# Performance work log

Measured on AMD Instinct MI355X. Metric: run time of the kernel, lower is better.

## Reference

```python
import jax, jax.numpy as jnp
import numpy as np

B, C, F_, T = 32, 2, 1024, 512
CF = C * F_
H = 128  # lstm hidden / embedding dim


def setup_inputs() -> dict:
    key = jax.random.key(0)
    ks = jax.random.split(key, 12)
    s = 0.05
    return {
        "x": jax.random.normal(ks[0], (B, C, F_, T), dtype=jnp.float32),
        "W_fc1": jax.random.normal(ks[1], (H, CF), dtype=jnp.float32) * s,
        "b_fc1": jax.random.normal(ks[2], (H,), dtype=jnp.float32) * s,
        "Wih_f": jax.random.normal(ks[3], (4 * H, H), dtype=jnp.float32) * s,
        "Whh_f": jax.random.normal(ks[4], (4 * H, H), dtype=jnp.float32) * s,
        "b_f": jax.random.normal(ks[5], (4 * H,), dtype=jnp.float32) * s,
        "Wih_b": jax.random.normal(ks[6], (4 * H, H), dtype=jnp.float32) * s,
        "Whh_b": jax.random.normal(ks[7], (4 * H, H), dtype=jnp.float32) * s,
        "b_b": jax.random.normal(ks[8], (4 * H,), dtype=jnp.float32) * s,
        "W_out": jax.random.normal(ks[9], (H, 2 * H), dtype=jnp.float32) * s,
        "b_out": jax.random.normal(ks[10], (H,), dtype=jnp.float32) * s,
    }


def _lstm_scan(x, Wih, Whh, b):
    # x: (L, T, H); recurrence over L (torch treats the (B,128) input as an
    # unbatched sequence of length B), vectorized over the T frames.
    L, Tn, _ = x.shape
    Hn = Whh.shape[1]

    def step(carry, xt):
        h, c = carry  # (T, H)
        z = xt @ Wih.T + h @ Whh.T + b  # (T, 4H)
        i, f, g, o = jnp.split(z, 4, axis=-1)
        c = jax.nn.sigmoid(f) * c + jax.nn.sigmoid(i) * jnp.tanh(g)
        h = jax.nn.sigmoid(o) * jnp.tanh(c)
        return (h, c), h

    init = (jnp.zeros((Tn, Hn), x.dtype), jnp.zeros((Tn, Hn), x.dtype))
    _, hs = jax.lax.scan(step, init, x)
    return hs  # (L, T, H)


def reference(x, W_fc1, b_fc1, Wih_f, Whh_f, b_f, Wih_b, Whh_b, b_b, W_out, b_out):
    Bn, Cn, Fn, Tn = x.shape
    # fc1 applied per time frame: (B, CF, T) -> (B, T, 128)
    xr = x.reshape(Bn, Cn * Fn, Tn).transpose(0, 2, 1)
    h = jnp.einsum("btc,dc->btd", xr, W_fc1) + b_fc1
    # bidirectional LSTM over the batch axis (torch unbatched-input semantics)
    hf = _lstm_scan(h, Wih_f, Whh_f, b_f)
    hb = _lstm_scan(h[::-1], Wih_b, Whh_b, b_b)[::-1]
    hs = jnp.concatenate([hf, hb], axis=-1)  # (B, T, 256)
    out = jnp.einsum("btd,ed->bte", hs, W_out) + b_out  # (B, T, 128)
    return out.transpose(0, 2, 1)  # (B, 128, T), matching torch.stack(dim=2)
```

## Files before the change

kernel.cpp:

```cpp
#include <hip/hip_runtime.h>
#include <stdint.h>

typedef __attribute__((ext_vector_type(8))) short short8;
typedef __attribute__((ext_vector_type(4))) float floatx4;

__device__ __forceinline__ float bf16_to_f(uint16_t u) {
    union { uint32_t i; float f; } v; v.i = ((uint32_t)u) << 16; return v.f;
}
__device__ __forceinline__ uint16_t f_to_bf16(float f) {
    union { uint32_t i; float f; } v; v.f = f;
    uint32_t u = v.i;
    u += 0x7FFFu + ((u >> 16) & 1u);
    return (uint16_t)(u >> 16);
}
__device__ __forceinline__ void gload16(const void* g, void* l) {
    __builtin_amdgcn_global_load_lds(
        (const __attribute__((address_space(1))) void*)g,
        (__attribute__((address_space(3))) void*)l, 16, 0, 0);
}
__device__ __forceinline__ float rcpf(float x) { return __builtin_amdgcn_rcpf(x); }

__device__ __forceinline__ void bar_lds() {
    asm volatile("s_waitcnt lgkmcnt(0)" ::: "memory");
    __builtin_amdgcn_s_barrier();
    asm volatile("" ::: "memory");
}

#define B_  32
#define T_  512
#define CF_ 2048
#define H_  128
#define G4_ 512
#define BT_ 16384
#define LOG2E 1.4426950408889634f

__global__ __launch_bounds__(256) void k_cvt_all(
        const float* __restrict__ Wfc, const float* __restrict__ Wih_f,
        const float* __restrict__ Wih_b, const float* __restrict__ Whh_f,
        const float* __restrict__ Whh_b, const float* __restrict__ Wout,
        uint16_t* __restrict__ WswzB, uint16_t* __restrict__ WihB,
        uint16_t* __restrict__ WhhB, uint16_t* __restrict__ WoutB) {
    const int blk = blockIdx.x;
    if (blk < 256) {
        const int i = blk * 1024 + threadIdx.x * 4;
        const int d = i >> 11, k = i & 2047;
        float4 v = *(const float4*)&Wfc[i];
        ushort4 o;
        o.x = f_to_bf16(v.x); o.y = f_to_bf16(v.y);
        o.z = f_to_bf16(v.z); o.w = f_to_bf16(v.w);
        const int kc = k >> 5, lk = (k >> 3) & 3, e = k & 7;
        const int mf = d >> 4, lm = d & 15;
        *(ushort4*)&WswzB[(size_t)(((kc * 8 + mf) * 64 + lk * 16 + lm) * 8 + e)] = o;
        return;
    }
    const float* s; uint16_t* d; int off;
    if (blk < 320)      { s = Wih_f; d = WihB;          off = blk - 256; }
    else if (blk < 384) { s = Wih_b; d = WihB + 65536;  off = blk - 320; }
    else if (blk < 448) { s = Whh_f; d = WhhB;          off = blk - 384; }
    else if (blk < 512) { s = Whh_b; d = WhhB + 65536;  off = blk - 448; }
    else                { s = Wout;  d = WoutB;         off = blk - 512; }
    const int i = off * 1024 + threadIdx.x * 4;
    float4 v = *(const float4*)&s[i];
    ushort4 o;
    o.x = f_to_bf16(v.x); o.y = f_to_bf16(v.y);
    o.z = f_to_bf16(v.z); o.w = f_to_bf16(v.w);
    *(ushort4*)&d[i] = o;
}

__global__ __launch_bounds__(256) void k_fc1w(const float* __restrict__ x,
                                              const uint16_t* __restrict__ Wswz,
                                              float* __restrict__ Hpart) {
    const int tid = threadIdx.x, w = tid >> 6, l = tid & 63;
    const int lm = l & 15, lk = l >> 4;
    const int bt0 = blockIdx.x * 16;
    const int bb = bt0 >> 9, t0 = bt0 & 511;
    const int kc4 = w;
    const float* xb = x + ((size_t)bb * CF_ + kc4 * 512) * T_ + t0 + lm;

    floatx4 acc[8] = {};
    #pragma unroll 2
    for (int s = 0; s < 16; ++s) {
        const int kk = s * 32;
        float xv[8];
        #pragma unroll
        for (int j = 0; j < 8; ++j)
            xv[j] = xb[(size_t)(kk + lk * 8 + j) * T_];
        short8 bfr;
        #pragma unroll
        for (int j = 0; j < 8; ++j)
            bfr[j] = (short)f_to_bf16(xv[j]);
        const uint16_t* wp = Wswz + ((size_t)(kc4 * 16 + s) * 8 * 64 + l) * 8;
        #pragma unroll
        for (int mf = 0; mf < 8; ++mf) {
            short8 a = *(const short8*)(wp + mf * 512);
            acc[mf] = __builtin_amdgcn_mfma_f32_16x16x32_bf16(a, bfr, acc[mf], 0, 0, 0);
        }
    }
    float* Hp = Hpart + (size_t)kc4 * H_ * BT_;
    #pragma unroll
    for (int mf = 0; mf < 8; ++mf) {
        const int d0 = mf * 16 + lk * 4;
        #pragma unroll
        for (int r = 0; r < 4; ++r)
            Hp[(size_t)(d0 + r) * BT_ + bt0 + lm] = acc[mf][r];
    }
}

__global__ __launch_bounds__(256) void k_hsum(const float* __restrict__ Hpart,
                                              const float* __restrict__ bfc,
                                              uint16_t* __restrict__ Hcm) {
    const int d = blockIdx.y, bt = blockIdx.x * 1024 + threadIdx.x * 4;
    const float b = bfc[d];
    float4 s = *(const float4*)&Hpart[(size_t)d * BT_ + bt];
    #pragma unroll
    for (int kc = 1; kc < 4; ++kc) {
        const float4 v = *(const float4*)&Hpart[(size_t)kc * H_ * BT_ + (size_t)d * BT_ + bt];
        s.x += v.x; s.y += v.y; s.z += v.z; s.w += v.w;
    }
    uint16_t* o = Hcm + ((size_t)(d >> 3) * BT_ + bt) * 8 + (d & 7);
    o[0]  = f_to_bf16(s.x + b);
    o[8]  = f_to_bf16(s.y + b);
    o[16] = f_to_bf16(s.z + b);
    o[24] = f_to_bf16(s.w + b);
}

__global__ __launch_bounds__(256) void k_xproj(const uint16_t* __restrict__ Hcm,
                                               const uint16_t* __restrict__ WihB,
                                               const float* __restrict__ b_f,
                                               const float* __restrict__ b_b,
                                               uint16_t* __restrict__ Xp) {
    __shared__ __align__(16) uint16_t As[64 * 136];
    __shared__ __align__(16) uint16_t Bs[16 * 66 * 8];
    const int bt0 = blockIdx.x * 64, gy = blockIdx.y;
    const int dir = gy >> 3;
    const int gl0 = gy * 64 - dir * 512;
    const int tid = threadIdx.x, w = tid >> 6, l = tid & 63;
    const int lm = l & 15, lk = l >> 4;

    #pragma unroll
    for (int j = 0; j < 4; ++j) {
        const int c = w * 4 + j;
        gload16(Hcm + ((size_t)c * BT_ + bt0 + l) * 8, Bs + (c * 66 + l) * 8);
    }
    {
        const int r = tid >> 2, c4 = tid & 3;
        const uint16_t* src = WihB + (size_t)(gy * 64 + r) * H_ + c4 * 32;
        short8 v0 = *(const short8*)(src);
        short8 v1 = *(const short8*)(src + 8);
        short8 v2 = *(const short8*)(src + 16);
        short8 v3 = *(const short8*)(src + 24);
        uint16_t* dst = &As[r * 136 + c4 * 32];
        *(short8*)(dst)      = v0;
        *(short8*)(dst + 8)  = v1;
        *(short8*)(dst + 16) = v2;
        *(short8*)(dst + 24) = v3;
    }
    __syncthreads();

    const int wm = (w >> 1) * 32, wn = (w & 1) * 32;
    short8 a[2][4], bfr[2][4];
    #pragma unroll
    for (int kf = 0; kf < 4; ++kf) {
        #pragma unroll
        for (int mf = 0; mf < 2; ++mf)
            a[mf][kf] = *(const short8*)&As[(wm + mf * 16 + lm) * 136 + kf * 32 + lk * 8];
        #pragma unroll
        for (int nf = 0; nf < 2; ++nf)
            bfr[nf][kf] = *(const short8*)&Bs[((kf * 4 + lk) * 66 + wn + nf * 16 + lm) * 8];
    }
    floatx4 acc[2][2] = {};
    #pragma unroll
    for (int kf = 0; kf < 4; ++kf)
        #pragma unroll
        for (int mf = 0; mf < 2; ++mf)
            #pragma unroll
            for (int nf = 0; nf < 2; ++nf)
                acc[mf][nf] = __builtin_amdgcn_mfma_f32_16x16x32_bf16(a[mf][kf], bfr[nf][kf], acc[mf][nf], 0, 0, 0);

    const float* bi = dir ? b_b : b_f;
    #pragma unroll
    for (int mf = 0; mf < 2; ++mf) {
        const int g = gl0 + wm + mf * 16 + lk * 4;
        const float4 bv = *(const float4*)&bi[g];
        #pragma unroll
        for (int nf = 0; nf < 2; ++nf) {
            const int bt = bt0 + wn + nf * 16 + lm;
            const int bb = bt >> 9, t = bt & 511;
            ushort4 o;
            o.x = f_to_bf16(acc[mf][nf][0] + bv.x);
            o.y = f_to_bf16(acc[mf][nf][1] + bv.y);
            o.z = f_to_bf16(acc[mf][nf][2] + bv.z);
            o.w = f_to_bf16(acc[mf][nf][3] + bv.w);
            *(ushort4*)&Xp[((size_t)(dir * B_ + bb) * T_ + t) * G4_ + g] = o;
        }
    }
}

__global__ __launch_bounds__(512) void k_lstm(const uint16_t* __restrict__ Xp,
                                              const uint16_t* __restrict__ WhhB,
                                              uint16_t* __restrict__ hs) {
    __shared__ __align__(16) uint16_t h_sh[2][16 * 136];
    const int dir = blockIdx.y, t0 = blockIdx.x * 16;
    const int tid = threadIdx.x, w = tid >> 6, l = tid & 63;
    const int lm = l & 15, lk = l >> 4;
    const int gcol = w * 16 + lm;
    const int tloc = lk * 4;
    const uint16_t* Wp = WhhB + dir * (G4_ * H_);

    short8 bw[4][4];
    #pragma unroll
    for (int q = 0; q < 4; ++q)
        #pragma unroll
        for (int kf = 0; kf < 4; ++kf)
            bw[q][kf] = *(const short8*)&Wp[(size_t)(q * H_ + gcol) * H_ + kf * 32 + lk * 8];

    for (int i = tid; i < 16 * 136; i += 512) h_sh[0][i] = 0;
    float c[4] = {0.f, 0.f, 0.f, 0.f};

    uint16_t xva[4][4], xvb[4][4];
    {
        const int b0 = dir ? (B_ - 1) : 0;
        const uint16_t* xp = Xp + ((size_t)(dir * B_ + b0) * T_ + t0 + tloc) * G4_;
        #pragma unroll
        for (int r = 0; r < 4; ++r)
            #pragma unroll
            for (int q = 0; q < 4; ++q)
                xva[r][q] = xp[(size_t)r * G4_ + q * H_ + gcol];
    }
    bar_lds();

    auto step = [&](int s, uint16_t (&xc)[4][4], uint16_t (&xn)[4][4], int par) {
        const int b_idx = dir ? (B_ - 1 - s) : s;
        short8 af[4];
        #pragma unroll
        for (int kf = 0; kf < 4; ++kf)
            af[kf] = *(const short8*)&h_sh[par][lm * 136 + kf * 32 + lk * 8];
        floatx4 acc[4] = {};
        #pragma unroll
        for (int q = 0; q < 4; ++q)
            #pragma unroll
            for (int kf = 0; kf < 4; ++kf)
                acc[q] = __builtin_amdgcn_mfma_f32_16x16x32_bf16(af[kf], bw[q][kf], acc[q], 0, 0, 0);
        if (s < B_ - 1) {
            const int bn = dir ? (B_ - 2 - s) : (s + 1);
            const uint16_t* xp = Xp + ((size_t)(dir * B_ + bn) * T_ + t0 + tloc) * G4_;
            #pragma unroll
            for (int r = 0; r < 4; ++r)
                #pragma unroll
                for (int q = 0; q < 4; ++q)
                    xn[r][q] = xp[(size_t)r * G4_ + q * H_ + gcol];
        }
        #pragma unroll
        for (int r = 0; r < 4; ++r) {
            float zi = acc[0][r] + bf16_to_f(xc[r][0]);
            float zf = acc[1][r] + bf16_to_f(xc[r][1]);
            float zg = acc[2][r] + bf16_to_f(xc[r][2]);
            float zo = acc[3][r] + bf16_to_f(xc[r][3]);
            float si = rcpf(1.f + __builtin_amdgcn_exp2f(-LOG2E * zi));
            float sf = rcpf(1.f + __builtin_amdgcn_exp2f(-LOG2E * zf));
            float so = rcpf(1.f + __builtin_amdgcn_exp2f(-LOG2E * zo));
            float tg = 1.f - 2.f * rcpf(1.f + __builtin_amdgcn_exp2f(2.f * LOG2E * zg));
            c[r] = sf * c[r] + si * tg;
            float tc = 1.f - 2.f * rcpf(1.f + __builtin_amdgcn_exp2f(2.f * LOG2E * c[r]));
            float hn = so * tc;
            uint16_t hb = f_to_bf16(hn);
            h_sh[par ^ 1][(tloc + r) * 136 + gcol] = hb;
            hs[((size_t)b_idx * T_ + t0 + tloc + r) * 256 + dir * H_ + gcol] = hb;
        }
        bar_lds();
    };

    for (int s2 = 0; s2 < 16; ++s2) {
        step(2 * s2,     xva, xvb, 0);
        step(2 * s2 + 1, xvb, xva, 1);
    }
}

__global__ __launch_bounds__(256) void k_outm(const uint16_t* __restrict__ WoutB,
                                              const uint16_t* __restrict__ hs,
                                              const float* __restrict__ bout,
                                              float* __restrict__ out) {
    __shared__ __align__(16) uint16_t As[4096], Bs[4096];
    const int b = blockIdx.z, m0 = blockIdx.y * 64, n0 = blockIdx.x * 64;
    const int tid = threadIdx.x, w = tid >> 6, l = tid & 63;
    const int wm = (w >> 1) * 32, wn = (w & 1) * 32;
    const int lm = l & 15, lk = l >> 4;
    const uint16_t* A = WoutB + (size_t)m0 * 256;
    const uint16_t* Bp = hs + ((size_t)b * T_ + n0) * 256;
    floatx4 acc[2][2] = {};
    const uint16_t* gA = A + (size_t)l * 256;
    const uint16_t* gB = Bp + (size_t)l * 256;
    for (int k0 = 0; k0 < 256; k0 += 64) {
        __syncthreads();
        gload16(gA + k0 + (2 * w) * 8,     As + ((2 * w) * 64 + l) * 8);
        gload16(gA + k0 + (2 * w + 1) * 8, As + ((2 * w + 1) * 64 + l) * 8);
        gload16(gB + k0 + (2 * w) * 8,     Bs + ((2 * w) * 64 + l) * 8);
        gload16(gB + k0 + (2 * w + 1) * 8, Bs + ((2 * w + 1) * 64 + l) * 8);
        __syncthreads();
        short8 a[2][2], bfr[2][2];
        #pragma unroll
        for (int kf = 0; kf < 2; ++kf) {
            #pragma unroll
            for (int mf = 0; mf < 2; ++mf)
                a[mf][kf] = *(const short8*)&As[((kf * 4 + lk) * 64 + wm + mf * 16 + lm) * 8];
            #pragma unroll
            for (int nf = 0; nf < 2; ++nf)
                bfr[nf][kf] = *(const short8*)&Bs[((kf * 4 + lk) * 64 + wn + nf * 16 + lm) * 8];
        }
        #pragma unroll
        for (int mf = 0; mf < 2; ++mf)
            #pragma unroll
            for (int nf = 0; nf < 2; ++nf) {
                acc[mf][nf] = __builtin_amdgcn_mfma_f32_16x16x32_bf16(a[mf][0], bfr[nf][0], acc[mf][nf], 0, 0, 0);
                acc[mf][nf] = __builtin_amdgcn_mfma_f32_16x16x32_bf16(a[mf][1], bfr[nf][1], acc[mf][nf], 0, 0, 0);
            }
    }
    #pragma unroll
    for (int mf = 0; mf < 2; ++mf) {
        const int e0 = m0 + wm + mf * 16 + lk * 4;
        const float4 bv = *(const float4*)&bout[e0];
        #pragma unroll
        for (int nf = 0; nf < 2; ++nf) {
            const int t = n0 + wn + nf * 16 + lm;
            out[((size_t)b * H_ + e0 + 0) * T_ + t] = acc[mf][nf][0] + bv.x;
            out[((size_t)b * H_ + e0 + 1) * T_ + t] = acc[mf][nf][1] + bv.y;
            out[((size_t)b * H_ + e0 + 2) * T_ + t] = acc[mf][nf][2] + bv.z;
            out[((size_t)b * H_ + e0 + 3) * T_ + t] = acc[mf][nf][3] + bv.w;
        }
    }
}

extern "C" void kernel_launch(void* const* d_in, const int* in_sizes, int n_in,
                              void* d_out, int out_size, void* d_ws, size_t ws_size,
                              hipStream_t stream) {
    const float* x     = (const float*)d_in[0];
    const float* Wfc   = (const float*)d_in[1];
    const float* bfc   = (const float*)d_in[2];
    const float* Wih_f = (const float*)d_in[3];
    const float* Whh_f = (const float*)d_in[4];
    const float* b_f   = (const float*)d_in[5];
    const float* Wih_b = (const float*)d_in[6];
    const float* Whh_b = (const float*)d_in[7];
    const float* b_b   = (const float*)d_in[8];
    const float* Wout  = (const float*)d_in[9];
    const float* bout  = (const float*)d_in[10];
    float* out = (float*)d_out;

    char* ws = (char*)d_ws;
    uint16_t* Xp    = (uint16_t*)(ws);
    uint16_t* hsB   = (uint16_t*)(ws + 33554432);
    float*    Hpart = (float*)   (ws + 41943040);
    uint16_t* Hcm   = (uint16_t*)(ws + 75497472);
    uint16_t* Wswz  = (uint16_t*)(ws + 79691776);
    uint16_t* WihB  = (uint16_t*)(ws + 80216064);
    uint16_t* WhhB  = (uint16_t*)(ws + 80478208);
    uint16_t* WoutB = (uint16_t*)(ws + 80740352);

    k_cvt_all<<<dim3(544), 256, 0, stream>>>(Wfc, Wih_f, Wih_b, Whh_f, Whh_b, Wout,
                                             Wswz, WihB, WhhB, WoutB);
    k_fc1w <<<dim3(1024),     256, 0, stream>>>(x, Wswz, Hpart);
    k_hsum <<<dim3(16, 128),  256, 0, stream>>>(Hpart, bfc, Hcm);
    k_xproj<<<dim3(256, 16),  256, 0, stream>>>(Hcm, WihB, b_f, b_b, Xp);
    k_lstm <<<dim3(32, 2),    512, 0, stream>>>(Xp, WhhB, hsB);
    k_outm <<<dim3(8, 2, 32), 256, 0, stream>>>(WoutB, hsB, bout, out);
}
```

Measured before the change: 332.5 us.

## Stage fc1 weight slices in LDS and widen per-wave time tile

The fc1 GEMM kernel now gives each block a 256-deep K-slice (8 splits) across 256 time frames. The block's 64KB bf16 weight slice is staged in LDS, and each wave computes 4 time fragments so every weight fragment feeds 4 MFMAs. The old kernel re-read weights from global memory for every 16-frame block. The cost is a larger partial-sum buffer (8 splits instead of 4) for the reduction kernel to sum, plus heavy LDS and register use (128 accumulator floats), which lowers occupancy.

```diff
diff --git a/kernel.cpp b/kernel.cpp
--- a/kernel.cpp
+++ b/kernel.cpp
@@ -67,42 +67,57 @@
     *(ushort4*)&d[i] = o;
 }
 
-__global__ __launch_bounds__(256) void k_fc1w(const float* __restrict__ x,
-                                              const uint16_t* __restrict__ Wswz,
-                                              float* __restrict__ Hpart) {
+__global__ __launch_bounds__(256) void k_fc1w2(const float* __restrict__ x,
+                                               const uint16_t* __restrict__ Wswz,
+                                               float* __restrict__ Hpart) {
+    __shared__ __align__(16) uint16_t Wl[32768];
     const int tid = threadIdx.x, w = tid >> 6, l = tid & 63;
     const int lm = l & 15, lk = l >> 4;
-    const int bt0 = blockIdx.x * 16;
+    const int bt0 = blockIdx.x * 256;
+    const int kc8 = blockIdx.y;
     const int bb = bt0 >> 9, t0 = bt0 & 511;
-    const int kc4 = w;
-    const float* xb = x + ((size_t)bb * CF_ + kc4 * 512) * T_ + t0 + lm;
-
-    floatx4 acc[8] = {};
+    const int btw = w * 64;
+
+    const uint16_t* wsrc = Wswz + (size_t)kc8 * 32768;
+    #pragma unroll
+    for (int it = 0; it < 16; ++it)
+        gload16(wsrc + (size_t)(it * 256 + tid) * 8, Wl + (it * 256 + tid) * 8);
+    __syncthreads();
+
+    const float* xb = x + ((size_t)bb * CF_ + kc8 * 256) * T_ + t0 + btw + lm;
+
+    floatx4 acc[8][4] = {};
     #pragma unroll 2
-    for (int s = 0; s < 16; ++s) {
+    for (int s = 0; s < 8; ++s) {
         const int kk = s * 32;
-        float xv[8];
-        #pragma unroll
-        for (int j = 0; j < 8; ++j)
-            xv[j] = xb[(size_t)(kk + lk * 8 + j) * T_];
-        short8 bfr;
-        #pragma unroll
-        for (int j = 0; j < 8; ++j)
-            bfr[j] = (short)f_to_bf16(xv[j]);
-        const uint16_t* wp = Wswz + ((size_t)(kc4 * 16 + s) * 8 * 64 + l) * 8;
+        short8 bfr[4];
+        #pragma unroll
+        for (int nf = 0; nf < 4; ++nf) {
+            float xv[8];
+            #pragma unroll
+            for (int j = 0; j < 8; ++j)
+                xv[j] = xb[(size_t)(kk + lk * 8 + j) * T_ + nf * 16];
+            #pragma unroll
+            for (int j = 0; j < 8; ++j)
+                bfr[nf][j] = (short)f_to_bf16(xv[j]);
+        }
         #pragma unroll
         for (int mf = 0; mf < 8; ++mf) {
-            short8 a = *(const short8*)(wp + mf * 512);
-            acc[mf] = __builtin_amdgcn_mfma_f32_16x16x32_bf16(a, bfr, acc[mf], 0, 0, 0);
-        }
-    }
-    float* Hp = Hpart + (size_t)kc4 * H_ * BT_;
+            const short8 a = *(const short8*)&Wl[((s * 8 + mf) * 64 + l) * 8];
+            #pragma unroll
+            for (int nf = 0; nf < 4; ++nf)
+                acc[mf][nf] = __builtin_amdgcn_mfma_f32_16x16x32_bf16(a, bfr[nf], acc[mf][nf], 0, 0, 0);
+        }
+    }
+    float* Hp = Hpart + (size_t)kc8 * H_ * BT_;
     #pragma unroll
     for (int mf = 0; mf < 8; ++mf) {
         const int d0 = mf * 16 + lk * 4;
         #pragma unroll
-        for (int r = 0; r < 4; ++r)
-            Hp[(size_t)(d0 + r) * BT_ + bt0 + lm] = acc[mf][r];
+        for (int nf = 0; nf < 4; ++nf)
+            #pragma unroll
+            for (int r = 0; r < 4; ++r)
+                Hp[(size_t)(d0 + r) * BT_ + bt0 + btw + nf * 16 + lm] = acc[mf][nf][r];
     }
 }
 
@@ -113,7 +128,7 @@
     const float b = bfc[d];
     float4 s = *(const float4*)&Hpart[(size_t)d * BT_ + bt];
     #pragma unroll
-    for (int kc = 1; kc < 4; ++kc) {
+    for (int kc = 1; kc < 8; ++kc) {
         const float4 v = *(const float4*)&Hpart[(size_t)kc * H_ * BT_ + (size_t)d * BT_ + bt];
         s.x += v.x; s.y += v.y; s.z += v.z; s.w += v.w;
     }
@@ -350,15 +365,15 @@
     uint16_t* Xp    = (uint16_t*)(ws);
     uint16_t* hsB   = (uint16_t*)(ws + 33554432);
     float*    Hpart = (float*)   (ws + 41943040);
-    uint16_t* Hcm   = (uint16_t*)(ws + 75497472);
-    uint16_t* Wswz  = (uint16_t*)(ws + 79691776);
-    uint16_t* WihB  = (uint16_t*)(ws + 80216064);
-    uint16_t* WhhB  = (uint16_t*)(ws + 80478208);
-    uint16_t* WoutB = (uint16_t*)(ws + 80740352);
+    uint16_t* Hcm   = (uint16_t*)(ws + 109051904);
+    uint16_t* Wswz  = (uint16_t*)(ws + 113246208);
+    uint16_t* WihB  = (uint16_t*)(ws + 113770496);
+    uint16_t* WhhB  = (uint16_t*)(ws + 114032640);
+    uint16_t* WoutB = (uint16_t*)(ws + 114294784);
 
     k_cvt_all<<<dim3(544), 256, 0, stream>>>(Wfc, Wih_f, Wih_b, Whh_f, Whh_b, Wout,
                                              Wswz, WihB, WhhB, WoutB);
-    k_fc1w <<<dim3(1024),     256, 0, stream>>>(x, Wswz, Hpart);
+    k_fc1w2<<<dim3(64, 8),    256, 0, stream>>>(x, Wswz, Hpart);
     k_hsum <<<dim3(16, 128),  256, 0, stream>>>(Hpart, bfc, Hcm);
     k_xproj<<<dim3(256, 16),  256, 0, stream>>>(Hcm, WihB, b_f, b_b, Xp);
     k_lstm <<<dim3(32, 2),    512, 0, stream>>>(Xp, WhhB, hsB);
```

Result: faster. 309.8 us (-6.8%).
